# Kernel tuning notes

Hardware: AMD Instinct MI355X
Metric: run time of the kernel (lower is better)

## Reference

```python
import jax, jax.numpy as jnp
import numpy as np

EPS = 1e-7
POS_THR = 0.5   # max_iou assigner positive threshold
NEG_THR = 0.4   # max_iou assigner negative threshold
ALPHA, GAMMA = 0.25, 2.0  # focal loss defaults


def _rand_boxes(key, shape):
    k1, k2 = jax.random.split(key)
    c = jax.random.uniform(k1, shape + (2,), minval=0.05, maxval=0.95)
    wh = jax.random.uniform(k2, shape + (2,), minval=0.02, maxval=0.3)
    return jnp.concatenate([jnp.clip(c - wh / 2, 0, 1), jnp.clip(c + wh / 2, 0, 1)], -1)


def _grid_anchors():
    # 3 anchor sizes per cell on 80x80, 40x40, 20x20 grids -> 25200 anchors, normalized coords
    boxes = []
    for g, sizes in [(80, (0.04, 0.08, 0.12)), (40, (0.1, 0.2, 0.3)), (20, (0.25, 0.45, 0.65))]:
        c = (np.arange(g, dtype=np.float32) + 0.5) / g
        cx, cy = np.meshgrid(c, c)
        for s in sizes:
            boxes.append(np.stack([cx - s / 2, cy - s / 2, cx + s / 2, cy + s / 2], -1).reshape(-1, 4))
    return jnp.asarray(np.concatenate(boxes, 0), dtype=jnp.float32)


def setup_inputs() -> dict:
    key = jax.random.key(0)
    ks = jax.random.split(key, 6)
    N, P, A, C = 32, 100, 25200, 80
    labels = jax.random.randint(ks[0], (N, P), 0, C)
    y_true = jax.nn.one_hot(labels, C, dtype=jnp.float32)
    bbox_true = _rand_boxes(ks[1], (N, P))
    valid = (jnp.arange(P)[None, :] < 30).astype(jnp.float32)  # 30 real boxes, rest zero-padded
    bbox_true = bbox_true * valid[..., None]
    conf_pred = jax.random.uniform(ks[2], (N, A, 1), minval=0.01, maxval=0.99)
    logit_pred = jax.random.uniform(ks[3], (N, A, C), minval=0.01, maxval=0.99)
    bbox_pred = _rand_boxes(ks[4], (N, A))
    anchors = _grid_anchors()
    return {"y_true": y_true, "bbox_true": bbox_true, "conf_pred": conf_pred,
            "logit_pred": logit_pred, "bbox_pred": bbox_pred, "anchors": anchors}


def pairwise_iou(a, b):
    # a: (A,4), b: (P,4) -> (A,P)
    iw = jnp.clip(jnp.minimum(a[:, None, 2], b[None, :, 2]) - jnp.maximum(a[:, None, 0], b[None, :, 0]), 0)
    ih = jnp.clip(jnp.minimum(a[:, None, 3], b[None, :, 3]) - jnp.maximum(a[:, None, 1], b[None, :, 1]), 0)
    inter = iw * ih
    area_a = (a[:, 2] - a[:, 0]) * (a[:, 3] - a[:, 1])
    area_b = (b[:, 2] - b[:, 0]) * (b[:, 3] - b[:, 1])
    return inter / (area_a[:, None] + area_b[None, :] - inter + EPS)


def target_single(y_true, bbox_true, anchors):
    # mask-based equivalent of the dynamic tf.where/gather/scatter target construction
    P = bbox_true.shape[0]
    valid = jnp.any(bbox_true > 0, axis=-1)  # (P,)
    iou = jnp.where(valid[None, :], pairwise_iou(anchors, bbox_true), -1.0)  # (A,P)
    max_iou = iou.max(-1)
    true_idx = iou.argmax(-1)
    pos = max_iou >= POS_THR
    neg = max_iou < NEG_THR
    # low-quality match: best anchor for each valid gt is positive
    gt_max = iou.max(0)
    gt_best = iou.argmax(0)
    lowq = valid & (gt_max > 0)
    pos = pos.astype(jnp.int32).at[gt_best].max(lowq.astype(jnp.int32)).astype(bool)
    true_idx = true_idx.at[gt_best].set(jnp.where(lowq, jnp.arange(P), true_idx[gt_best]))
    neg = neg & ~pos
    state = jnp.where(pos, 1, jnp.where(neg, -1, 0)).astype(jnp.int8)
    C = y_true.shape[-1]
    background = jnp.zeros((C,), jnp.float32).at[0].set(1.0)  # tf.pad(ones,[0,C-1]) default
    tgt_label = jnp.where(pos[:, None], y_true[true_idx], background[None, :])
    tgt_bbox = jnp.where(pos[:, None], bbox_true[true_idx], 0.0)
    return state[:, None], tgt_label, tgt_bbox


def ciou_loss(bt, bp):
    ix1 = jnp.maximum(bt[..., 0], bp[..., 0]); iy1 = jnp.maximum(bt[..., 1], bp[..., 1])
    ix2 = jnp.minimum(bt[..., 2], bp[..., 2]); iy2 = jnp.minimum(bt[..., 3], bp[..., 3])
    inter = jnp.clip(ix2 - ix1, 0) * jnp.clip(iy2 - iy1, 0)
    wt, ht = bt[..., 2] - bt[..., 0], bt[..., 3] - bt[..., 1]
    wp, hp = bp[..., 2] - bp[..., 0], bp[..., 3] - bp[..., 1]
    union = wt * ht + wp * hp - inter + EPS
    iou = inter / union
    cw = jnp.maximum(bt[..., 2], bp[..., 2]) - jnp.minimum(bt[..., 0], bp[..., 0])
    ch = jnp.maximum(bt[..., 3], bp[..., 3]) - jnp.minimum(bt[..., 1], bp[..., 1])
    c2 = cw * cw + ch * ch + EPS
    rho2 = ((bt[..., 0] + bt[..., 2] - bp[..., 0] - bp[..., 2]) ** 2 +
            (bt[..., 1] + bt[..., 3] - bp[..., 1] - bp[..., 3]) ** 2) / 4.0
    v = (4.0 / (np.pi ** 2)) * (jnp.arctan(wt / (ht + EPS)) - jnp.arctan(wp / (hp + EPS))) ** 2
    alpha = jax.lax.stop_gradient(v / (1.0 - iou + v + EPS))
    return 1.0 - iou + rho2 / c2 + alpha * v


def reference(y_true, bbox_true, conf_pred, logit_pred, bbox_pred, anchors):
    state, t_label, t_bbox = jax.vmap(target_single, in_axes=(0, 0, None))(y_true, bbox_true, anchors)
    dtype = logit_pred.dtype
    pw = (state == 1).astype(dtype)   # positive_weight (N,A,1)
    tw = (state != 0).astype(dtype)   # target_weight   (N,A,1)
    avg_factor = jnp.sum(jnp.maximum(jnp.sum(pw, axis=-2), 1.0))
    # score loss: BCE(positive_weight, conf_pred), weighted by target_weight
    p = jnp.clip(conf_pred, EPS, 1.0 - EPS)
    score_l = -(pw * jnp.log(p) + (1.0 - pw) * jnp.log(1.0 - p))
    score_l = jnp.sum(score_l * tw) / avg_factor
    # class loss: focal BCE, weighted by positive_weight
    q = jnp.clip(logit_pred, EPS, 1.0 - EPS)
    pt = t_label * q + (1.0 - t_label) * (1.0 - q)
    at = t_label * ALPHA + (1.0 - t_label) * (1.0 - ALPHA)
    cls_l = -at * (1.0 - pt) ** GAMMA * jnp.log(pt)
    cls_l = jnp.sum(cls_l * pw) / avg_factor
    # bbox loss: CIoU, weighted by positive_weight
    bl = ciou_loss(t_bbox, bbox_pred)[..., None]
    bbox_l = jnp.sum(bl * pw) / avg_factor
    guard = lambda x: jnp.where(jnp.isnan(x) | jnp.isinf(x), jnp.zeros_like(x), x)  # missing_value=0
    return guard(score_l), guard(cls_l), guard(bbox_l)
```

## Files before the change

### kernel.cpp

```cpp
#include <hip/hip_runtime.h>
#include <math.h>

#define EPSF 1e-7f

__device__ __forceinline__ float iou_pair(const float4 a, const float4 b) {
    float iw = fminf(a.z, b.z) - fmaxf(a.x, b.x); iw = iw > 0.f ? iw : 0.f;
    float ih = fminf(a.w, b.w) - fmaxf(a.y, b.y); ih = ih > 0.f ? ih : 0.f;
    float inter = iw * ih;
    float aa = (a.z - a.x) * (a.w - a.y);
    float ab = (b.z - b.x) * (b.w - b.y);
    return inter / (aa + ab - inter + EPSF);
}

__global__ __launch_bounds__(256) void k_gt(const float4* __restrict__ bbox_true,
                                            const float4* __restrict__ anchors,
                                            float* __restrict__ gt_max,
                                            int* __restrict__ gt_best,
                                            int P, int A) {
    int p = blockIdx.x, n = blockIdx.y;
    float4 b = bbox_true[(size_t)n * P + p];
    bool valid = (b.x > 0.f || b.y > 0.f || b.z > 0.f || b.w > 0.f);
    if (!valid) {
        if (threadIdx.x == 0) { gt_max[n * P + p] = -1.f; gt_best[n * P + p] = 0; }
        return;
    }
    float best = -2.f; int bi = 0x7fffffff;
    for (int a = threadIdx.x; a < A; a += blockDim.x) {
        float iou = iou_pair(anchors[a], b);
        if (iou > best) { best = iou; bi = a; }
    }
    __shared__ float sv[256];
    __shared__ int   si[256];
    int tid = threadIdx.x;
    sv[tid] = best; si[tid] = bi;
    __syncthreads();
    for (int s = 128; s > 0; s >>= 1) {
        if (tid < s) {
            if (sv[tid + s] > sv[tid] ||
                (sv[tid + s] == sv[tid] && si[tid + s] < si[tid])) {
                sv[tid] = sv[tid + s]; si[tid] = si[tid + s];
            }
        }
        __syncthreads();
    }
    if (tid == 0) { gt_max[n * P + p] = sv[0]; gt_best[n * P + p] = si[0]; }
}

__global__ void k_scatter(const float* __restrict__ gt_max,
                          const int* __restrict__ gt_best,
                          int* __restrict__ ovr,
                          int N, int P, int A) {
    int n = blockIdx.x * blockDim.x + threadIdx.x;
    if (n >= N) return;
    for (int p = 0; p < P; p++) {
        int idx = gt_best[n * P + p];
        size_t o = (size_t)n * A + idx;
        if (gt_max[n * P + p] > 0.f) {
            ovr[o] = p;
        } else {
            int cur = ovr[o];
            if (cur != -1) ovr[o] = -2;
        }
    }
}

__global__ __launch_bounds__(256) void k_fused(const float4* __restrict__ bbox_true,
                                               const float4* __restrict__ anchors,
                                               const float* __restrict__ conf,
                                               const float* __restrict__ logit,
                                               const float4* __restrict__ bbox_pred,
                                               const float* __restrict__ y_true,
                                               const int* __restrict__ ovr,
                                               double* __restrict__ partial,
                                               int P, int A, int C, int BX) {
    int tid = threadIdx.x;
    int n = blockIdx.y;
    int a = blockIdx.x * blockDim.x + tid;

    __shared__ float4 scb[256];
    __shared__ int    sidx[256];
    __shared__ int    wcnt[4];

    float4 b = make_float4(0.f, 0.f, 0.f, 0.f);
    bool v = false;
    if (tid < P) {
        b = bbox_true[(size_t)n * P + tid];
        v = (b.x > 0.f || b.y > 0.f || b.z > 0.f || b.w > 0.f);
    }
    unsigned long long m = __ballot(v);
    int lane = tid & 63, wv = tid >> 6;
    if (lane == 0) wcnt[wv] = __popcll(m);
    int posn = __popcll(m & ((1ull << lane) - 1ull));
    __syncthreads();
    int base = 0;
    for (int w = 0; w < wv; w++) base += wcnt[w];
    int V = wcnt[0] + wcnt[1] + wcnt[2] + wcnt[3];
    if (v) { scb[base + posn] = b; sidx[base + posn] = tid; }
    __syncthreads();

    double sc = 0.0, cl = 0.0, bb = 0.0, pc = 0.0;
    if (a < A) {
        float4 an = anchors[a];
        float best = -2.f; int bi = 0;
        for (int k = 0; k < V; k++) {
            float iou = iou_pair(an, scb[k]);
            if (iou > best) { best = iou; bi = sidx[k]; }
        }
        if (V == 0) best = -1.f;
        size_t o = (size_t)n * A + a;
        int ov = ovr[o];
        bool pos = (best >= 0.5f) || (ov != -1);
        bool neg = (best < 0.4f) && !pos;
        int t = (ov >= 0) ? ov : bi;

        float p = conf[o];
        p = fminf(fmaxf(p, EPSF), 1.f - EPSF);
        if (pos || neg) sc = (double)(pos ? -logf(p) : -logf(1.f - p));
        if (pos) {
            pc = 1.0;
            const float* yt = y_true + ((size_t)n * P + t) * C;
            const float* lg = logit + o * C;
            float s = 0.f;
            for (int c = 0; c < C; c++) {
                float tl = yt[c];
                float q = fminf(fmaxf(lg[c], EPSF), 1.f - EPSF);
                float pt = tl * q + (1.f - tl) * (1.f - q);
                float at = tl * 0.25f + (1.f - tl) * 0.75f;
                float om = 1.f - pt;
                s += -at * om * om * logf(pt);
            }
            cl = (double)s;
            float4 bt = bbox_true[(size_t)n * P + t];
            float4 bp = bbox_pred[o];
            float ix1 = fmaxf(bt.x, bp.x), iy1 = fmaxf(bt.y, bp.y);
            float ix2 = fminf(bt.z, bp.z), iy2 = fminf(bt.w, bp.w);
            float iw = ix2 - ix1; iw = iw > 0.f ? iw : 0.f;
            float ih = iy2 - iy1; ih = ih > 0.f ? ih : 0.f;
            float inter = iw * ih;
            float wt = bt.z - bt.x, ht = bt.w - bt.y;
            float wp = bp.z - bp.x, hp = bp.w - bp.y;
            float uni = wt * ht + wp * hp - inter + EPSF;
            float iou = inter / uni;
            float cw = fmaxf(bt.z, bp.z) - fminf(bt.x, bp.x);
            float ch = fmaxf(bt.w, bp.w) - fminf(bt.y, bp.y);
            float c2 = cw * cw + ch * ch + EPSF;
            float dx = bt.x + bt.z - bp.x - bp.z;
            float dy = bt.y + bt.w - bp.y - bp.w;
            float rho2 = (dx * dx + dy * dy) * 0.25f;
            float dd = atanf(wt / (ht + EPSF)) - atanf(wp / (hp + EPSF));
            float vv = 0.40528473456935109f * dd * dd;
            float al = vv / (1.f - iou + vv + EPSF);
            bb = (double)(1.f - iou + rho2 / c2 + al * vv);
        }
    }

    for (int off = 32; off > 0; off >>= 1) {
        sc += __shfl_down(sc, off, 64);
        cl += __shfl_down(cl, off, 64);
        bb += __shfl_down(bb, off, 64);
        pc += __shfl_down(pc, off, 64);
    }
    __shared__ double sred[4][4];
    if (lane == 0) { sred[wv][0] = sc; sred[wv][1] = cl; sred[wv][2] = bb; sred[wv][3] = pc; }
    __syncthreads();
    if (tid == 0) {
        double r0 = 0, r1 = 0, r2 = 0, r3 = 0;
        for (int w = 0; w < 4; w++) {
            r0 += sred[w][0]; r1 += sred[w][1]; r2 += sred[w][2]; r3 += sred[w][3];
        }
        double* row = partial + ((size_t)n * BX + blockIdx.x) * 4;
        row[0] = r0; row[1] = r1; row[2] = r2; row[3] = r3;
    }
}

__global__ __launch_bounds__(256) void k_final(const double* __restrict__ partial,
                                               float* __restrict__ out, int N, int BX) {
    const int FT = 256;
    int tid = threadIdx.x;
    __shared__ double sh[FT];
    __shared__ double res[3];
    __shared__ double shn[64];

    double s0 = 0, s1 = 0, s2 = 0;
    int total = N * BX;
    for (int i = tid; i < total; i += FT) {
        const double* r = partial + (size_t)i * 4;
        s0 += r[0]; s1 += r[1]; s2 += r[2];
    }
    double vals[3] = {s0, s1, s2};
    for (int k = 0; k < 3; k++) {
        sh[tid] = vals[k];
        __syncthreads();
        for (int s = 128; s > 0; s >>= 1) {
            if (tid < s) sh[tid] += sh[tid + s];
            __syncthreads();
        }
        if (tid == 0) res[k] = sh[0];
        __syncthreads();
    }
    int chunks = FT / N;
    double pcs = 0;
    int n = tid / chunks, c = tid % chunks;
    if (n < N) {
        int per = (BX + chunks - 1) / chunks;
        int j0 = c * per, j1 = (j0 + per < BX) ? j0 + per : BX;
        for (int j = j0; j < j1; j++) pcs += partial[((size_t)n * BX + j) * 4 + 3];
    }
    sh[tid] = pcs;
    __syncthreads();
    if (tid < N) {
        double s = 0;
        for (int c2 = 0; c2 < chunks; c2++) s += sh[tid * chunks + c2];
        shn[tid] = s > 1.0 ? s : 1.0;
    }
    __syncthreads();
    if (tid == 0) {
        double avg = 0;
        for (int i = 0; i < N; i++) avg += shn[i];
        for (int k = 0; k < 3; k++) {
            double x = res[k] / avg;
            if (isnan(x) || isinf(x)) x = 0.0;
            out[k] = (float)x;
        }
    }
}

extern "C" void kernel_launch(void* const* d_in, const int* in_sizes, int n_in,
                              void* d_out, int out_size, void* d_ws, size_t ws_size,
                              hipStream_t stream) {
    const float* y_true    = (const float*)d_in[0];
    const float* bbox_true = (const float*)d_in[1];
    const float* conf      = (const float*)d_in[2];
    const float* logit     = (const float*)d_in[3];
    const float* bboxp     = (const float*)d_in[4];
    const float* anchors   = (const float*)d_in[5];

    int A = in_sizes[5] / 4;
    int N = in_sizes[2] / A;
    int P = in_sizes[1] / (4 * N);
    int C = in_sizes[0] / (N * P);

    int BX = (A + 255) / 256;

    char* w = (char*)d_ws;
    auto alloc = [&](size_t bytes) -> void* {
        void* r = (void*)w;
        w += (bytes + 15) & ~(size_t)15;
        return r;
    };
    int*    ovr     = (int*)alloc(sizeof(int) * (size_t)N * A);
    float*  gt_max  = (float*)alloc(sizeof(float) * (size_t)N * P);
    int*    gt_best = (int*)alloc(sizeof(int) * (size_t)N * P);
    double* partial = (double*)alloc(sizeof(double) * (size_t)N * BX * 4);

    hipMemsetAsync(ovr, 0xFF, sizeof(int) * (size_t)N * A, stream);

    dim3 gG(P, N);
    k_gt<<<gG, 256, 0, stream>>>((const float4*)bbox_true, (const float4*)anchors,
                                 gt_max, gt_best, P, A);

    k_scatter<<<(N + 63) / 64, 64, 0, stream>>>(gt_max, gt_best, ovr, N, P, A);

    dim3 gA(BX, N);
    k_fused<<<gA, 256, 0, stream>>>((const float4*)bbox_true, (const float4*)anchors,
                                    conf, logit, (const float4*)bboxp, y_true,
                                    ovr, partial, P, A, C, BX);

    k_final<<<1, 256, 0, stream>>>(partial, (float*)d_out, N, BX);
}
```

Measured before the change: 445.5 us.

## Segment per-GT argmax over anchors, batch GTs per block, parallelize scatter

Replaces the per-(GT, image) block that scanned all anchors with blocks that each own an anchor segment. Each block processes up to 10 GT boxes per anchor load, comparing IoU as numerator/denominator cross-products to avoid divides, then merges segment winners in a new per-image kernel. That kernel also replaces the serial per-image scatter loop with a parallel last-writer resolution. The fused kernel likewise drops the IoU division in favour of cross-multiplied comparisons. The intent is to cut redundant anchor reloads, divides and the serial scatter, at the cost of extra workspace, more shared memory and a possible tie-break or rounding difference from the divide-free comparisons.

Result: slower. 523.8 us (+17.6%).

```diff
diff --git a/kernel.cpp b/kernel.cpp
--- a/kernel.cpp
+++ b/kernel.cpp
@@ -2,65 +2,141 @@
 #include <math.h>
 
 #define EPSF 1e-7f
-
-__device__ __forceinline__ float iou_pair(const float4 a, const float4 b) {
-    float iw = fminf(a.z, b.z) - fmaxf(a.x, b.x); iw = iw > 0.f ? iw : 0.f;
-    float ih = fminf(a.w, b.w) - fmaxf(a.y, b.y); ih = ih > 0.f ? ih : 0.f;
-    float inter = iw * ih;
-    float aa = (a.z - a.x) * (a.w - a.y);
-    float ab = (b.z - b.x) * (b.w - b.y);
-    return inter / (aa + ab - inter + EPSF);
-}
-
-__global__ __launch_bounds__(256) void k_gt(const float4* __restrict__ bbox_true,
-                                            const float4* __restrict__ anchors,
-                                            float* __restrict__ gt_max,
-                                            int* __restrict__ gt_best,
-                                            int P, int A) {
-    int p = blockIdx.x, n = blockIdx.y;
-    float4 b = bbox_true[(size_t)n * P + p];
-    bool valid = (b.x > 0.f || b.y > 0.f || b.z > 0.f || b.w > 0.f);
-    if (!valid) {
-        if (threadIdx.x == 0) { gt_max[n * P + p] = -1.f; gt_best[n * P + p] = 0; }
-        return;
-    }
-    float best = -2.f; int bi = 0x7fffffff;
-    for (int a = threadIdx.x; a < A; a += blockDim.x) {
-        float iou = iou_pair(anchors[a], b);
-        if (iou > best) { best = iou; bi = a; }
-    }
-    __shared__ float sv[256];
-    __shared__ int   si[256];
-    int tid = threadIdx.x;
-    sv[tid] = best; si[tid] = bi;
-    __syncthreads();
-    for (int s = 128; s > 0; s >>= 1) {
-        if (tid < s) {
-            if (sv[tid + s] > sv[tid] ||
-                (sv[tid + s] == sv[tid] && si[tid + s] < si[tid])) {
-                sv[tid] = sv[tid + s]; si[tid] = si[tid + s];
-            }
-        }
-        __syncthreads();
-    }
-    if (tid == 0) { gt_max[n * P + p] = sv[0]; gt_best[n * P + p] = si[0]; }
-}
-
-__global__ void k_scatter(const float* __restrict__ gt_max,
-                          const int* __restrict__ gt_best,
-                          int* __restrict__ ovr,
-                          int N, int P, int A) {
-    int n = blockIdx.x * blockDim.x + threadIdx.x;
-    if (n >= N) return;
-    for (int p = 0; p < P; p++) {
-        int idx = gt_best[n * P + p];
-        size_t o = (size_t)n * A + idx;
-        if (gt_max[n * P + p] > 0.f) {
-            ovr[o] = p;
-        } else {
-            int cur = ovr[o];
-            if (cur != -1) ovr[o] = -2;
-        }
+#define GCHUNK 10
+#define NSEG 8
+
+__device__ __forceinline__ int compact_valid(const float4* __restrict__ bt_n, int P, int tid,
+                                             float4* scb, int* sidx, float* sarea, int* wcnt) {
+    float4 b = make_float4(0.f, 0.f, 0.f, 0.f);
+    bool v = false;
+    if (tid < P) {
+        b = bt_n[tid];
+        v = (b.x > 0.f || b.y > 0.f || b.z > 0.f || b.w > 0.f);
+    }
+    unsigned long long m = __ballot(v);
+    int lane = tid & 63, wv = tid >> 6;
+    if (lane == 0) wcnt[wv] = __popcll(m);
+    int posn = __popcll(m & ((1ull << lane) - 1ull));
+    __syncthreads();
+    int base = 0;
+    for (int w = 0; w < wv; w++) base += wcnt[w];
+    int V = wcnt[0] + wcnt[1] + wcnt[2] + wcnt[3];
+    if (v) {
+        scb[base + posn] = b;
+        sidx[base + posn] = tid;
+        sarea[base + posn] = (b.z - b.x) * (b.w - b.y);
+    }
+    __syncthreads();
+    return V;
+}
+
+__global__ __launch_bounds__(256) void k_gt_seg(const float4* __restrict__ bbox_true,
+                                                const float4* __restrict__ anchors,
+                                                float* __restrict__ pn, float* __restrict__ pd,
+                                                int* __restrict__ pi,
+                                                int N, int P, int A) {
+    __shared__ float4 scb[256];
+    __shared__ int    sidx[256];
+    __shared__ float  sarea[256];
+    __shared__ int    wcnt[4];
+    __shared__ float  sn[256 * GCHUNK];
+    __shared__ float  sd[256 * GCHUNK];
+    __shared__ int    si[256 * GCHUNK];
+
+    int n = blockIdx.y, seg = blockIdx.x, tid = threadIdx.x;
+    int V = compact_valid(bbox_true + (size_t)n * P, P, tid, scb, sidx, sarea, wcnt);
+    int len = (A + NSEG - 1) / NSEG;
+    int a0 = seg * len;
+    int a1 = a0 + len < A ? a0 + len : A;
+
+    for (int c0 = 0; c0 < V; c0 += GCHUNK) {
+        int G = V - c0 < GCHUNK ? V - c0 : GCHUNK;
+        float bn[GCHUNK], bd[GCHUNK];
+        int   bi[GCHUNK];
+#pragma unroll
+        for (int g = 0; g < GCHUNK; g++) { bn[g] = -1.f; bd[g] = 1.f; bi[g] = 0x7fffffff; }
+        for (int a = a0 + tid; a < a1; a += 256) {
+            float4 an = anchors[a];
+            float aa = (an.z - an.x) * (an.w - an.y);
+#pragma unroll
+            for (int g = 0; g < GCHUNK; g++) {
+                if (g < G) {
+                    float4 b = scb[c0 + g];
+                    float iw = fminf(an.z, b.z) - fmaxf(an.x, b.x); iw = iw > 0.f ? iw : 0.f;
+                    float ih = fminf(an.w, b.w) - fmaxf(an.y, b.y); ih = ih > 0.f ? ih : 0.f;
+                    float inter = iw * ih;
+                    float den = aa + sarea[c0 + g] - inter + EPSF;
+                    if (inter * bd[g] > bn[g] * den) { bn[g] = inter; bd[g] = den; bi[g] = a; }
+                }
+            }
+        }
+        __syncthreads();
+#pragma unroll
+        for (int g = 0; g < GCHUNK; g++) {
+            sn[tid * GCHUNK + g] = bn[g];
+            sd[tid * GCHUNK + g] = bd[g];
+            si[tid * GCHUNK + g] = bi[g];
+        }
+        __syncthreads();
+        if (tid < G) {
+            float Bn = -1.f, Bd = 1.f; int Bi = 0x7fffffff;
+            for (int i = 0; i < 256; i++) {
+                float cn = sn[i * GCHUNK + tid], cd = sd[i * GCHUNK + tid];
+                int ci = si[i * GCHUNK + tid];
+                if (cn >= 0.f) {
+                    float l = cn * Bd, r = Bn * cd;
+                    if (l > r || (l == r && ci < Bi)) { Bn = cn; Bd = cd; Bi = ci; }
+                }
+            }
+            int p = sidx[c0 + tid];
+            size_t o = ((size_t)n * P + p) * NSEG + seg;
+            pn[o] = Bn; pd[o] = Bd; pi[o] = Bi;
+        }
+        __syncthreads();
+    }
+}
+
+__global__ __launch_bounds__(128) void k_merge_scatter(const float4* __restrict__ bbox_true,
+                                                       const float* __restrict__ pn,
+                                                       const float* __restrict__ pd,
+                                                       const int* __restrict__ pi,
+                                                       int* __restrict__ ovr,
+                                                       int N, int P, int A) {
+    int n = blockIdx.x, p = threadIdx.x;
+    __shared__ int gb[128];
+    __shared__ unsigned char lqs[128];
+    if (p < P) {
+        float4 b = bbox_true[(size_t)n * P + p];
+        bool valid = (b.x > 0.f || b.y > 0.f || b.z > 0.f || b.w > 0.f);
+        int g = 0; bool lq = false;
+        if (valid) {
+            float Bn = -1.f, Bd = 1.f; int Bi = 0x7fffffff;
+            const float* qn = pn + ((size_t)n * P + p) * NSEG;
+            const float* qd = pd + ((size_t)n * P + p) * NSEG;
+            const int*   qi = pi + ((size_t)n * P + p) * NSEG;
+            for (int s = 0; s < NSEG; s++) {
+                float cn = qn[s], cd = qd[s]; int ci = qi[s];
+                if (cn >= 0.f) {
+                    float l = cn * Bd, r = Bn * cd;
+                    if (l > r || (l == r && ci < Bi)) { Bn = cn; Bd = cd; Bi = ci; }
+                }
+            }
+            g = Bi;
+            lq = (Bn > 0.f);
+        }
+        gb[p] = g; lqs[p] = lq ? 1 : 0;
+    }
+    __syncthreads();
+    if (p < P) {
+        int myidx = gb[p];
+        bool anylq = false, islast = true;
+        for (int q = 0; q < P; q++) {
+            if (gb[q] == myidx) {
+                if (lqs[q]) anylq = true;
+                if (q > p) islast = false;
+            }
+        }
+        if (islast && anylq) ovr[(size_t)n * A + myidx] = lqs[p] ? p : -2;
     }
 }
 
@@ -76,41 +152,35 @@
     int tid = threadIdx.x;
     int n = blockIdx.y;
     int a = blockIdx.x * blockDim.x + tid;
+    int lane = tid & 63, wv = tid >> 6;
 
     __shared__ float4 scb[256];
     __shared__ int    sidx[256];
+    __shared__ float  sarea[256];
     __shared__ int    wcnt[4];
 
-    float4 b = make_float4(0.f, 0.f, 0.f, 0.f);
-    bool v = false;
-    if (tid < P) {
-        b = bbox_true[(size_t)n * P + tid];
-        v = (b.x > 0.f || b.y > 0.f || b.z > 0.f || b.w > 0.f);
-    }
-    unsigned long long m = __ballot(v);
-    int lane = tid & 63, wv = tid >> 6;
-    if (lane == 0) wcnt[wv] = __popcll(m);
-    int posn = __popcll(m & ((1ull << lane) - 1ull));
-    __syncthreads();
-    int base = 0;
-    for (int w = 0; w < wv; w++) base += wcnt[w];
-    int V = wcnt[0] + wcnt[1] + wcnt[2] + wcnt[3];
-    if (v) { scb[base + posn] = b; sidx[base + posn] = tid; }
-    __syncthreads();
+    int V = compact_valid(bbox_true + (size_t)n * P, P, tid, scb, sidx, sarea, wcnt);
 
     double sc = 0.0, cl = 0.0, bb = 0.0, pc = 0.0;
     if (a < A) {
         float4 an = anchors[a];
-        float best = -2.f; int bi = 0;
+        float aa = (an.z - an.x) * (an.w - an.y);
+        float bn = -1.f, bd = 1.f; int bi = 0;
         for (int k = 0; k < V; k++) {
-            float iou = iou_pair(an, scb[k]);
-            if (iou > best) { best = iou; bi = sidx[k]; }
-        }
-        if (V == 0) best = -1.f;
+            float4 b = scb[k];
+            float iw = fminf(an.z, b.z) - fmaxf(an.x, b.x); iw = iw > 0.f ? iw : 0.f;
+            float ih = fminf(an.w, b.w) - fmaxf(an.y, b.y); ih = ih > 0.f ? ih : 0.f;
+            float inter = iw * ih;
+            float den = aa + sarea[k] - inter + EPSF;
+            if (inter * bd > bn * den) { bn = inter; bd = den; bi = sidx[k]; }
+        }
+        bool pos, neg;
+        if (V > 0) { pos = (bn >= 0.5f * bd); neg = (bn < 0.4f * bd); }
+        else       { pos = false; neg = true; }
         size_t o = (size_t)n * A + a;
         int ov = ovr[o];
-        bool pos = (best >= 0.5f) || (ov != -1);
-        bool neg = (best < 0.4f) && !pos;
+        pos = pos || (ov != -1);
+        neg = neg && !pos;
         int t = (ov >= 0) ? ov : bi;
 
         float p = conf[o];
@@ -249,17 +319,19 @@
         return r;
     };
     int*    ovr     = (int*)alloc(sizeof(int) * (size_t)N * A);
-    float*  gt_max  = (float*)alloc(sizeof(float) * (size_t)N * P);
-    int*    gt_best = (int*)alloc(sizeof(int) * (size_t)N * P);
+    float*  pn      = (float*)alloc(sizeof(float) * (size_t)N * P * NSEG);
+    float*  pd      = (float*)alloc(sizeof(float) * (size_t)N * P * NSEG);
+    int*    pi      = (int*)alloc(sizeof(int) * (size_t)N * P * NSEG);
     double* partial = (double*)alloc(sizeof(double) * (size_t)N * BX * 4);
 
     hipMemsetAsync(ovr, 0xFF, sizeof(int) * (size_t)N * A, stream);
 
-    dim3 gG(P, N);
-    k_gt<<<gG, 256, 0, stream>>>((const float4*)bbox_true, (const float4*)anchors,
-                                 gt_max, gt_best, P, A);
-
-    k_scatter<<<(N + 63) / 64, 64, 0, stream>>>(gt_max, gt_best, ovr, N, P, A);
+    dim3 gS(NSEG, N);
+    k_gt_seg<<<gS, 256, 0, stream>>>((const float4*)bbox_true, (const float4*)anchors,
+                                     pn, pd, pi, N, P, A);
+
+    k_merge_scatter<<<N, 128, 0, stream>>>((const float4*)bbox_true, pn, pd, pi,
+                                           ovr, N, P, A);
 
     dim3 gA(BX, N);
     k_fused<<<gA, 256, 0, stream>>>((const float4*)bbox_true, (const float4*)anchors,
```
